# Optimization experiments

Hardware: AMD Instinct MI355X
Metric: run time of the kernel (lower is better)

Reference implementation:

```python
import jax, jax.numpy as jnp
import numpy as np

B = 1_048_576
IN_DIM, OUT_DIM, H = 64, 64, 32
EPS = 1e-5
SLOPE = 0.01  # nn.LeakyReLU default negative_slope


def setup_inputs() -> dict:
    key = jax.random.key(0)
    ks = jax.random.split(key, 25)
    r = lambda k, shp, s=0.05: jax.random.normal(k, shp, dtype=jnp.float32) * s
    return {
        "x": jax.random.normal(ks[0], (B, IN_DIM), dtype=jnp.float32),
        # layer1: Linear(in_dim, 32)
        "w1": r(ks[1], (IN_DIM, H)), "b1": r(ks[2], (H,)),
        # attention1 (Self_Attn1D): q/k project to H//8, v to H, scalar gamma
        "wq1": r(ks[3], (H, H // 8)), "bq1": r(ks[4], (H // 8,)),
        "wk1": r(ks[5], (H, H // 8)), "bk1": r(ks[6], (H // 8,)),
        "wv1": r(ks[7], (H, H)), "bv1": r(ks[8], (H,)),
        "g1": r(ks[9], (1,), 0.1),
        "ln1_g": 1.0 + r(ks[10], (H,)), "ln1_b": r(ks[11], (H,)),
        # layer2: Linear(32, 32)
        "w2": r(ks[12], (H, H)), "b2": r(ks[13], (H,)),
        # attention2
        "wq2": r(ks[14], (H, H // 8)), "bq2": r(ks[15], (H // 8,)),
        "wk2": r(ks[16], (H, H // 8)), "bk2": r(ks[17], (H // 8,)),
        "wv2": r(ks[18], (H, H)), "bv2": r(ks[19], (H,)),
        "g2": r(ks[20], (1,), 0.1),
        "ln2_g": 1.0 + r(ks[21], (H,)), "ln2_b": r(ks[22], (H,)),
        # output: Linear(32, out_dim)
        "wo": r(ks[23], (H, OUT_DIM)), "bo": r(ks[24], (OUT_DIM,)),
    }


def _self_attn_1d(x, wq, bq, wk, bk, wv, bv, gamma):
    # x: [B, C] is treated as a length-1 sequence [B, C, T=1] (SAGAN-style 1D attn).
    q = (x @ wq + bq)[:, None, :]              # [B, 1, C//8]
    k = (x @ wk + bk)[:, None, :]              # [B, 1, C//8]
    energy = jnp.einsum('btc,bsc->bts', q, k)  # [B, 1, 1]
    attn = jax.nn.softmax(energy, axis=-1)     # exactly ones for T=1
    v = (x @ wv + bv)[:, None, :]              # [B, 1, C]
    out = jnp.einsum('bts,bsc->btc', attn, v)[:, 0]  # [B, C]
    return gamma * out + x


def _layer_norm(x, g, b):
    m = jnp.mean(x, axis=-1, keepdims=True)
    v = jnp.var(x, axis=-1, keepdims=True)
    return (x - m) * jax.lax.rsqrt(v + EPS) * g + b


def _leaky_relu(x):
    return jnp.where(x >= 0, x, SLOPE * x)


def reference(x, w1, b1, wq1, bq1, wk1, bk1, wv1, bv1, g1, ln1_g, ln1_b,
              w2, b2, wq2, bq2, wk2, bk2, wv2, bv2, g2, ln2_g, ln2_b, wo, bo):
    h = x.astype(jnp.float32) @ w1 + b1
    h = _self_attn_1d(h, wq1, bq1, wk1, bk1, wv1, bv1, g1)
    h = _leaky_relu(_layer_norm(h, ln1_g, ln1_b))
    h = h @ w2 + b2
    h = _self_attn_1d(h, wq2, bq2, wk2, bk2, wv2, bv2, g2)
    h = _leaky_relu(_layer_norm(h, ln2_g, ln2_b))
    return h @ wo + bo
```

## Files before the change

kernel.cpp:

```cpp
#include <hip/hip_runtime.h>


#define HDIM 32
#define EPS 1e-5f
#define SLOPE 0.01f


__global__ void mlp_preproc(
    const float* __restrict__ w1, const float* __restrict__ b1,
    const float* __restrict__ wv1, const float* __restrict__ bv1,
    const float* __restrict__ g1,
    const float* __restrict__ w2, const float* __restrict__ b2,
    const float* __restrict__ wv2, const float* __restrict__ bv2,
    const float* __restrict__ g2,
    const float* __restrict__ wo, const float* __restrict__ bo,
    float* __restrict__ ws)
{
    const int t = threadIdx.x;
    const float gg1 = g1[0], gg2 = g2[0];

    for (int e = t; e < 64 * HDIM; e += 256) {
        int k = e >> 5, j = e & 31;
        float acc = 0.f;
        for (int m = 0; m < HDIM; ++m) acc += w1[k * HDIM + m] * wv1[m * HDIM + j];
        ws[e] = w1[e] + gg1 * acc;
    }
    if (t < HDIM) {
        int j = t;
        float s = 0.f;
        for (int m = 0; m < HDIM; ++m) s += b1[m] * wv1[m * HDIM + j];
        ws[2048 + j] = b1[j] + gg1 * (s + bv1[j]);
    }
    for (int e = t; e < HDIM * HDIM; e += 256) {
        int k = e >> 5, j = e & 31;
        float acc = 0.f;
        for (int m = 0; m < HDIM; ++m) acc += w2[k * HDIM + m] * wv2[m * HDIM + j];
        ws[2080 + e] = w2[e] + gg2 * acc;
    }
    if (t < HDIM) {
        int j = t;
        float s = 0.f;
        for (int m = 0; m < HDIM; ++m) s += b2[m] * wv2[m * HDIM + j];
        ws[3104 + j] = b2[j] + gg2 * (s + bv2[j]);
    }
    for (int e = t; e < 64 * HDIM; e += 256) {
        int j = e >> 5, k = e & 31;
        ws[3136 + e] = wo[k * 64 + j];
    }
    if (t < 64) ws[5184 + t] = bo[t];
}

__global__ __launch_bounds__(256, 4) void mlp_main(
    const float* __restrict__ x,
    const float* __restrict__ ws,
    const float* __restrict__ ln1g, const float* __restrict__ ln1b,
    const float* __restrict__ ln2g, const float* __restrict__ ln2b,
    float* __restrict__ out)
{
    const int row = blockIdx.x * 256 + threadIdx.x;

    const float* __restrict__ W1f = ws;
    const float* __restrict__ B1f = ws + 2048;
    const float* __restrict__ W2f = ws + 2080;
    const float* __restrict__ B2f = ws + 3104;
    const float* __restrict__ WoT = ws + 3136;
    const float* __restrict__ Bo  = ws + 5184;

    const float4* __restrict__ xr = (const float4*)(x + (size_t)row * 64);

    float h1[HDIM];
#pragma unroll
    for (int j = 0; j < HDIM; ++j) h1[j] = B1f[j];

#pragma unroll 1
    for (int c = 0; c < 4; ++c) {
        alignas(16) float q[16];
        *(float4*)&q[0]  = xr[c * 4 + 0];
        *(float4*)&q[4]  = xr[c * 4 + 1];
        *(float4*)&q[8]  = xr[c * 4 + 2];
        *(float4*)&q[12] = xr[c * 4 + 3];
        const float* __restrict__ wb = W1f + c * 512;
#pragma unroll
        for (int kk = 0; kk < 16; ++kk) {
            const float xk = q[kk];
#pragma unroll
            for (int j = 0; j < HDIM; ++j)
                h1[j] = fmaf(xk, wb[kk * HDIM + j], h1[j]);
        }
    }

    {
        float m = 0.f;
#pragma unroll
        for (int j = 0; j < HDIM; ++j) m += h1[j];
        m *= (1.f / HDIM);
        float v = 0.f;
#pragma unroll
        for (int j = 0; j < HDIM; ++j) { float t = h1[j] - m; v = fmaf(t, t, v); }
        v *= (1.f / HDIM);
        const float rs = rsqrtf(v + EPS);
#pragma unroll
        for (int j = 0; j < HDIM; ++j) {
            float a = (h1[j] - m) * rs * ln1g[j] + ln1b[j];
            h1[j] = (a >= 0.f) ? a : SLOPE * a;
        }
    }

    float h2[HDIM];
#pragma unroll
    for (int j = 0; j < HDIM; ++j) h2[j] = B2f[j];
#pragma unroll
    for (int k = 0; k < HDIM; ++k) {
        const float hk = h1[k];
#pragma unroll
        for (int j = 0; j < HDIM; ++j)
            h2[j] = fmaf(hk, W2f[k * HDIM + j], h2[j]);
    }

    {
        float m = 0.f;
#pragma unroll
        for (int j = 0; j < HDIM; ++j) m += h2[j];
        m *= (1.f / HDIM);
        float v = 0.f;
#pragma unroll
        for (int j = 0; j < HDIM; ++j) { float t = h2[j] - m; v = fmaf(t, t, v); }
        v *= (1.f / HDIM);
        const float rs = rsqrtf(v + EPS);
#pragma unroll
        for (int j = 0; j < HDIM; ++j) {
            float a = (h2[j] - m) * rs * ln2g[j] + ln2b[j];
            h2[j] = (a >= 0.f) ? a : SLOPE * a;
        }
    }

    float4* __restrict__ outr = (float4*)(out + (size_t)row * 64);
#pragma unroll 1
    for (int c = 0; c < 4; ++c) {
        float acc[16];
#pragma unroll
        for (int jj = 0; jj < 16; ++jj) acc[jj] = Bo[c * 16 + jj];
        const float* __restrict__ wb = WoT + c * 512;
#pragma unroll
        for (int jj = 0; jj < 16; ++jj) {
#pragma unroll
            for (int k = 0; k < HDIM; ++k)
                acc[jj] = fmaf(h2[k], wb[jj * HDIM + k], acc[jj]);
        }
        float4 o0 = { acc[0],  acc[1],  acc[2],  acc[3]  };
        float4 o1 = { acc[4],  acc[5],  acc[6],  acc[7]  };
        float4 o2 = { acc[8],  acc[9],  acc[10], acc[11] };
        float4 o3 = { acc[12], acc[13], acc[14], acc[15] };
        outr[c * 4 + 0] = o0;
        outr[c * 4 + 1] = o1;
        outr[c * 4 + 2] = o2;
        outr[c * 4 + 3] = o3;
    }
}

extern "C" void kernel_launch(void* const* d_in, const int* in_sizes, int n_in,
                              void* d_out, int out_size, void* d_ws, size_t ws_size,
                              hipStream_t stream) {
    const float* x    = (const float*)d_in[0];
    const float* w1   = (const float*)d_in[1];
    const float* b1   = (const float*)d_in[2];
    const float* wv1  = (const float*)d_in[7];
    const float* bv1  = (const float*)d_in[8];
    const float* g1   = (const float*)d_in[9];
    const float* ln1g = (const float*)d_in[10];
    const float* ln1b = (const float*)d_in[11];
    const float* w2   = (const float*)d_in[12];
    const float* b2   = (const float*)d_in[13];
    const float* wv2  = (const float*)d_in[18];
    const float* bv2  = (const float*)d_in[19];
    const float* g2   = (const float*)d_in[20];
    const float* ln2g = (const float*)d_in[21];
    const float* ln2b = (const float*)d_in[22];
    const float* wo   = (const float*)d_in[23];
    const float* bo   = (const float*)d_in[24];

    float* ws = (float*)d_ws;
    float* out = (float*)d_out;

    const int rows = in_sizes[0] / 64;

    mlp_preproc<<<1, 256, 0, stream>>>(w1, b1, wv1, bv1, g1,
                                       w2, b2, wv2, bv2, g2,
                                       wo, bo, ws);

    mlp_main<<<rows / 256, 256, 0, stream>>>(x, ws, ln1g, ln1b, ln2g, ln2b, out);
}
```

Measured before the change: 619.6 us.

## Use packed float2 math throughout main kernel and read wo directly

Rewrites all three matmuls and both layernorm stages with two-wide float vectors so the compiler can emit packed FP32 FMA instructions (v_pk_fma_f32) on CDNA. It also drops the transposed wo copy in the preprocessing kernel and reads wo/bo in its native row-major layout, which suits the packed output layout. The occupancy hint moves from launch_bounds min-blocks to amdgpu_waves_per_eu(4,4). Packing may add register shuffles for broadcasts and can change register allocation.

```diff
diff --git a/kernel.cpp b/kernel.cpp
--- a/kernel.cpp
+++ b/kernel.cpp
@@ -4,6 +4,8 @@
 #define HDIM 32
 #define EPS 1e-5f
 #define SLOPE 0.01f
+
+typedef float v2f __attribute__((ext_vector_type(2)));
 
 
 __global__ void mlp_preproc(
@@ -13,7 +15,6 @@
     const float* __restrict__ w2, const float* __restrict__ b2,
     const float* __restrict__ wv2, const float* __restrict__ bv2,
     const float* __restrict__ g2,
-    const float* __restrict__ wo, const float* __restrict__ bo,
     float* __restrict__ ws)
 {
     const int t = threadIdx.x;
@@ -43,34 +44,36 @@
         for (int m = 0; m < HDIM; ++m) s += b2[m] * wv2[m * HDIM + j];
         ws[3104 + j] = b2[j] + gg2 * (s + bv2[j]);
     }
-    for (int e = t; e < 64 * HDIM; e += 256) {
-        int j = e >> 5, k = e & 31;
-        ws[3136 + e] = wo[k * 64 + j];
-    }
-    if (t < 64) ws[5184 + t] = bo[t];
 }
 
-__global__ __launch_bounds__(256, 4) void mlp_main(
+__global__ __launch_bounds__(256)
+__attribute__((amdgpu_waves_per_eu(4, 4)))
+void mlp_main(
     const float* __restrict__ x,
     const float* __restrict__ ws,
     const float* __restrict__ ln1g, const float* __restrict__ ln1b,
     const float* __restrict__ ln2g, const float* __restrict__ ln2b,
+    const float* __restrict__ wo,   const float* __restrict__ bo,
     float* __restrict__ out)
 {
     const int row = blockIdx.x * 256 + threadIdx.x;
 
-    const float* __restrict__ W1f = ws;
-    const float* __restrict__ B1f = ws + 2048;
-    const float* __restrict__ W2f = ws + 2080;
-    const float* __restrict__ B2f = ws + 3104;
-    const float* __restrict__ WoT = ws + 3136;
-    const float* __restrict__ Bo  = ws + 5184;
+    const v2f* __restrict__ W1v = (const v2f*)ws;
+    const v2f* __restrict__ B1v = (const v2f*)(ws + 2048);
+    const v2f* __restrict__ W2v = (const v2f*)(ws + 2080);
+    const v2f* __restrict__ B2v = (const v2f*)(ws + 3104);
+    const v2f* __restrict__ WoV = (const v2f*)wo;
+    const v2f* __restrict__ BoV = (const v2f*)bo;
+    const v2f* __restrict__ G1  = (const v2f*)ln1g;
+    const v2f* __restrict__ Bt1 = (const v2f*)ln1b;
+    const v2f* __restrict__ G2  = (const v2f*)ln2g;
+    const v2f* __restrict__ Bt2 = (const v2f*)ln2b;
 
     const float4* __restrict__ xr = (const float4*)(x + (size_t)row * 64);
 
-    float h1[HDIM];
-#pragma unroll
-    for (int j = 0; j < HDIM; ++j) h1[j] = B1f[j];
+    v2f h1[16];
+#pragma unroll
+    for (int j = 0; j < 16; ++j) h1[j] = B1v[j];
 
 #pragma unroll 1
     for (int c = 0; c < 4; ++c) {
@@ -79,78 +82,92 @@
         *(float4*)&q[4]  = xr[c * 4 + 1];
         *(float4*)&q[8]  = xr[c * 4 + 2];
         *(float4*)&q[12] = xr[c * 4 + 3];
-        const float* __restrict__ wb = W1f + c * 512;
+        const v2f* __restrict__ wb = W1v + c * 256;
 #pragma unroll
         for (int kk = 0; kk < 16; ++kk) {
-            const float xk = q[kk];
-#pragma unroll
-            for (int j = 0; j < HDIM; ++j)
-                h1[j] = fmaf(xk, wb[kk * HDIM + j], h1[j]);
+            const v2f xk2 = { q[kk], q[kk] };
+#pragma unroll
+            for (int j = 0; j < 16; ++j)
+                h1[j] = h1[j] + xk2 * wb[kk * 16 + j];
         }
     }
 
     {
-        float m = 0.f;
-#pragma unroll
-        for (int j = 0; j < HDIM; ++j) m += h1[j];
-        m *= (1.f / HDIM);
-        float v = 0.f;
-#pragma unroll
-        for (int j = 0; j < HDIM; ++j) { float t = h1[j] - m; v = fmaf(t, t, v); }
-        v *= (1.f / HDIM);
-        const float rs = rsqrtf(v + EPS);
-#pragma unroll
-        for (int j = 0; j < HDIM; ++j) {
-            float a = (h1[j] - m) * rs * ln1g[j] + ln1b[j];
-            h1[j] = (a >= 0.f) ? a : SLOPE * a;
-        }
-    }
-
-    float h2[HDIM];
-#pragma unroll
-    for (int j = 0; j < HDIM; ++j) h2[j] = B2f[j];
-#pragma unroll
-    for (int k = 0; k < HDIM; ++k) {
-        const float hk = h1[k];
-#pragma unroll
-        for (int j = 0; j < HDIM; ++j)
-            h2[j] = fmaf(hk, W2f[k * HDIM + j], h2[j]);
+        v2f s = { 0.f, 0.f };
+#pragma unroll
+        for (int j = 0; j < 16; ++j) s = s + h1[j];
+        const float m = (s.x + s.y) * (1.f / HDIM);
+        const v2f mm = { m, m };
+        v2f vs = { 0.f, 0.f };
+#pragma unroll
+        for (int j = 0; j < 16; ++j) { v2f t = h1[j] - mm; vs = vs + t * t; }
+        const float rs = rsqrtf((vs.x + vs.y) * (1.f / HDIM) + EPS);
+        const v2f rsv = { rs, rs };
+#pragma unroll
+        for (int j = 0; j < 16; ++j) {
+            v2f a = (h1[j] - mm) * rsv * G1[j] + Bt1[j];
+            a.x = fmaxf(a.x, SLOPE * a.x);
+            a.y = fmaxf(a.y, SLOPE * a.y);
+            h1[j] = a;
+        }
+    }
+
+    v2f h2[16];
+#pragma unroll
+    for (int j = 0; j < 16; ++j) h2[j] = B2v[j];
+#pragma unroll
+    for (int i = 0; i < 16; ++i) {
+        const v2f hx = { h1[i].x, h1[i].x };
+        const v2f hy = { h1[i].y, h1[i].y };
+        const v2f* __restrict__ w0 = W2v + (2 * i) * 16;
+        const v2f* __restrict__ w1r = W2v + (2 * i + 1) * 16;
+#pragma unroll
+        for (int j = 0; j < 16; ++j) h2[j] = h2[j] + hx * w0[j];
+#pragma unroll
+        for (int j = 0; j < 16; ++j) h2[j] = h2[j] + hy * w1r[j];
     }
 
     {
-        float m = 0.f;
-#pragma unroll
-        for (int j = 0; j < HDIM; ++j) m += h2[j];
-        m *= (1.f / HDIM);
-        float v = 0.f;
-#pragma unroll
-        for (int j = 0; j < HDIM; ++j) { float t = h2[j] - m; v = fmaf(t, t, v); }
-        v *= (1.f / HDIM);
-        const float rs = rsqrtf(v + EPS);
-#pragma unroll
-        for (int j = 0; j < HDIM; ++j) {
-            float a = (h2[j] - m) * rs * ln2g[j] + ln2b[j];
-            h2[j] = (a >= 0.f) ? a : SLOPE * a;
+        v2f s = { 0.f, 0.f };
+#pragma unroll
+        for (int j = 0; j < 16; ++j) s = s + h2[j];
+        const float m = (s.x + s.y) * (1.f / HDIM);
+        const v2f mm = { m, m };
+        v2f vs = { 0.f, 0.f };
+#pragma unroll
+        for (int j = 0; j < 16; ++j) { v2f t = h2[j] - mm; vs = vs + t * t; }
+        const float rs = rsqrtf((vs.x + vs.y) * (1.f / HDIM) + EPS);
+        const v2f rsv = { rs, rs };
+#pragma unroll
+        for (int j = 0; j < 16; ++j) {
+            v2f a = (h2[j] - mm) * rsv * G2[j] + Bt2[j];
+            a.x = fmaxf(a.x, SLOPE * a.x);
+            a.y = fmaxf(a.y, SLOPE * a.y);
+            h2[j] = a;
         }
     }
 
     float4* __restrict__ outr = (float4*)(out + (size_t)row * 64);
 #pragma unroll 1
     for (int c = 0; c < 4; ++c) {
-        float acc[16];
-#pragma unroll
-        for (int jj = 0; jj < 16; ++jj) acc[jj] = Bo[c * 16 + jj];
-        const float* __restrict__ wb = WoT + c * 512;
-#pragma unroll
-        for (int jj = 0; jj < 16; ++jj) {
-#pragma unroll
-            for (int k = 0; k < HDIM; ++k)
-                acc[jj] = fmaf(h2[k], wb[jj * HDIM + k], acc[jj]);
-        }
-        float4 o0 = { acc[0],  acc[1],  acc[2],  acc[3]  };
-        float4 o1 = { acc[4],  acc[5],  acc[6],  acc[7]  };
-        float4 o2 = { acc[8],  acc[9],  acc[10], acc[11] };
-        float4 o3 = { acc[12], acc[13], acc[14], acc[15] };
+        v2f acc[8];
+#pragma unroll
+        for (int j = 0; j < 8; ++j) acc[j] = BoV[c * 8 + j];
+#pragma unroll
+        for (int i = 0; i < 16; ++i) {
+            const v2f hx = { h2[i].x, h2[i].x };
+            const v2f hy = { h2[i].y, h2[i].y };
+            const v2f* __restrict__ w0 = WoV + (2 * i) * 32 + c * 8;
+            const v2f* __restrict__ w1r = WoV + (2 * i + 1) * 32 + c * 8;
+#pragma unroll
+            for (int j = 0; j < 8; ++j) acc[j] = acc[j] + hx * w0[j];
+#pragma unroll
+            for (int j = 0; j < 8; ++j) acc[j] = acc[j] + hy * w1r[j];
+        }
+        float4 o0 = { acc[0].x, acc[0].y, acc[1].x, acc[1].y };
+        float4 o1 = { acc[2].x, acc[2].y, acc[3].x, acc[3].y };
+        float4 o2 = { acc[4].x, acc[4].y, acc[5].x, acc[5].y };
+        float4 o3 = { acc[6].x, acc[6].y, acc[7].x, acc[7].y };
         outr[c * 4 + 0] = o0;
         outr[c * 4 + 1] = o1;
         outr[c * 4 + 2] = o2;
@@ -185,8 +202,8 @@
     const int rows = in_sizes[0] / 64;
 
     mlp_preproc<<<1, 256, 0, stream>>>(w1, b1, wv1, bv1, g1,
-                                       w2, b2, wv2, bv2, g2,
-                                       wo, bo, ws);
-
-    mlp_main<<<rows / 256, 256, 0, stream>>>(x, ws, ln1g, ln1b, ln2g, ln2b, out);
+                                       w2, b2, wv2, bv2, g2, ws);
+
+    mlp_main<<<rows / 256, 256, 0, stream>>>(x, ws, ln1g, ln1b, ln2g, ln2b,
+                                             wo, bo, out);
 }
```

Measured after the change: 613.0 us. About the same (-1.1%).
